# Optimization experiments

Hardware: AMD Instinct MI355X
Metric: run time of the kernel (lower is better)

Reference implementation:

```python
import jax, jax.numpy as jnp
import numpy as np

N = 50000   # nodes
E = 800000  # edges
F = 64      # node_feature_dim
H = 128     # hidden_dim


def setup_inputs() -> dict:
    key = jax.random.key(0)
    ks = jax.random.split(key, 20)
    def w(k, shape, fan_in):
        return jax.random.normal(k, shape, jnp.float32) / np.sqrt(fan_in)
    return {
        "x": jax.random.normal(ks[0], (N, F), jnp.float32),
        "edge_index": jax.random.randint(ks[1], (2, E), 0, N, jnp.int32),
        "enc_w1": w(ks[2], (F, H), F), "enc_b1": jnp.zeros((H,), jnp.float32),
        "enc_w2": w(ks[3], (H, H), H), "enc_b2": jnp.zeros((H,), jnp.float32),
        "w_c1": w(ks[4], (H, H), H), "b_c1": jnp.zeros((H,), jnp.float32),
        "w_c2": w(ks[5], (H, H), H), "b_c2": jnp.zeros((H,), jnp.float32),
        "w_c3": w(ks[6], (H, H), H), "b_c3": jnp.zeros((H,), jnp.float32),
        "dec_w1": w(ks[7], (H, H), H), "dec_b1": jnp.zeros((H,), jnp.float32),
        "dec_w2": w(ks[8], (H, F), H), "dec_b2": jnp.zeros((F,), jnp.float32),
    }


def _gcn_conv(h, W, b, src, dst, dinv):
    # PyG GCNConv: D^-1/2 (A+I) D^-1/2 (h W) + b  (self-loops already in src/dst)
    hw = h @ W                                   # [N, H]
    norm = dinv[src] * dinv[dst]                 # [E+N]
    msg = hw[src] * norm[:, None]                # gather + scale
    return jax.ops.segment_sum(msg, dst, num_segments=N) + b


def reference(x, edge_index, enc_w1, enc_b1, enc_w2, enc_b2,
              w_c1, b_c1, w_c2, b_c2, w_c3, b_c3,
              dec_w1, dec_b1, dec_w2, dec_b2):
    loop = jnp.arange(N, dtype=edge_index.dtype)
    src = jnp.concatenate([edge_index[0], loop])
    dst = jnp.concatenate([edge_index[1], loop])
    deg = jax.ops.segment_sum(jnp.ones_like(dst, jnp.float32), dst, num_segments=N)
    dinv = jax.lax.rsqrt(deg)  # deg >= 1 because of self-loops

    h = jax.nn.relu(x @ enc_w1 + enc_b1) @ enc_w2 + enc_b2  # encoder MLP
    h = jax.nn.relu(_gcn_conv(h, w_c1, b_c1, src, dst, dinv))
    h = jax.nn.relu(_gcn_conv(h, w_c2, b_c2, src, dst, dinv))
    h = jax.nn.relu(_gcn_conv(h, w_c3, b_c3, src, dst, dinv))
    # window_size == 1: chunk+cat is identity
    out = jax.nn.relu(h @ dec_w1 + dec_b1) @ dec_w2 + dec_b2  # decoder MLP
    return jax.nn.sigmoid(out)
```

## Files before the change

### kernel.cpp

```cpp
#include <hip/hip_runtime.h>
#include <stdint.h>

#define NN 50000
#define NE 800000
#define FD 64
#define HD 128
#define NBKT 196
#define BCAP 5120
#define P1E 8192

static_assert(NN % 16 == 0, "aggm16 grid is exact");

typedef __attribute__((ext_vector_type(8))) short short8;
typedef __attribute__((ext_vector_type(4))) float f32x4;

#define AS1 __attribute__((address_space(1)))
#define AS3 __attribute__((address_space(3)))

__device__ __forceinline__ float bflo(unsigned int v) {
    union { unsigned int u; float f; } c; c.u = v << 16; return c.f;
}
__device__ __forceinline__ float bfhi(unsigned int v) {
    union { unsigned int u; float f; } c; c.u = v & 0xffff0000u; return c.f;
}
__device__ __forceinline__ unsigned short f2bf(float f) {
    union { float f; unsigned int u; } c; c.f = f;
    unsigned int u = c.u;
    return (unsigned short)((u + 0x7fffu + ((u >> 16) & 1u)) >> 16);
}
__device__ __forceinline__ unsigned int pack2(float a, float b) {
    return (unsigned int)f2bf(a) | ((unsigned int)f2bf(b) << 16);
}

__global__ void wt0_k(const float* __restrict__ w0, unsigned short* __restrict__ t0) {
    int e = blockIdx.x * 256 + threadIdx.x;
    int k = e >> 7, c = e & 127;
    int gsw = (k >> 3) ^ (c & 7);
    t0[c * 64 + gsw * 8 + (k & 7)] = f2bf(w0[e]);
}

template <int K, int COLS, int EPI, bool BIAS, bool RSCALE, bool A_F32, bool OUT_F32>
__device__ __forceinline__ void mgemm_dev(
    int bid,
    const void* __restrict__ Av,
    const unsigned short* __restrict__ Wt,
    const float* __restrict__ bias,
    const float* __restrict__ dinv,
    void* __restrict__ outv, int nrows)
{
    constexpr int NB = COLS / 16;
    constexpr int KC = K / 32;
    constexpr int GMASK = (K >> 3) - 1;
    __shared__ __align__(16) unsigned char Ws8[COLS * K * 2];

    const int tid = threadIdx.x;
    const int wave = tid >> 6;
    const int lane = tid & 63;

    {
        constexpr int ROUNDS = COLS * K * 2 / 4096;
        const int gb = wave * 1024 + lane * 16;
        const int lb = wave * 1024;
        #pragma unroll
        for (int r = 0; r < ROUNDS; r++) {
            __builtin_amdgcn_global_load_lds(
                (const AS1 unsigned int*)((const unsigned char*)Wt + r * 4096 + gb),
                (AS3 unsigned int*)(Ws8 + r * 4096 + lb),
                16, 0, 0);
        }
    }

    const int m = lane & 15;
    const int q = lane >> 4;
    const int row0 = bid * 64 + wave * 16;

    f32x4 acc[NB];
    #pragma unroll
    for (int i = 0; i < NB; i++) acc[i] = (f32x4){0.f, 0.f, 0.f, 0.f};

    const bool arow_ok = !A_F32 || (row0 + m) < nrows;

    short8 af[KC];
    #pragma unroll
    for (int kc = 0; kc < KC; kc++) {
        if constexpr (A_F32) {
            const float* arowf = (const float*)Av + (size_t)(row0 + m) * K + q * 8 + kc * 32;
            float4 lo = make_float4(0.f, 0.f, 0.f, 0.f), hi = lo;
            if (arow_ok) { lo = *(const float4*)arowf; hi = *(const float4*)(arowf + 4); }
            af[kc][0] = (short)f2bf(lo.x); af[kc][1] = (short)f2bf(lo.y);
            af[kc][2] = (short)f2bf(lo.z); af[kc][3] = (short)f2bf(lo.w);
            af[kc][4] = (short)f2bf(hi.x); af[kc][5] = (short)f2bf(hi.y);
            af[kc][6] = (short)f2bf(hi.z); af[kc][7] = (short)f2bf(hi.w);
        } else {
            const unsigned short* arow = (const unsigned short*)Av + (size_t)(row0 + m) * K + q * 8 + kc * 32;
            af[kc] = *(const short8*)arow;
        }
    }
    __syncthreads();

    #pragma unroll
    for (int kc = 0; kc < KC; kc++) {
        #pragma unroll
        for (int nb = 0; nb < NB; nb++) {
            const int c = nb * 16 + m;
            const int gsw = (kc * 4 + q) ^ (c & GMASK);
            short8 bf = *(const short8*)&Ws8[(c * K + gsw * 8) * 2];
            acc[nb] = __builtin_amdgcn_mfma_f32_16x16x32_bf16(af[kc], bf, acc[nb], 0, 0, 0);
        }
    }

    float bv[NB];
    #pragma unroll
    for (int nb = 0; nb < NB; nb++) bv[nb] = BIAS ? bias[nb * 16 + m] : 0.f;

    #pragma unroll
    for (int r = 0; r < 4; r++) {
        int row = row0 + q * 4 + r;
        if (row < nrows) {
            float sc = RSCALE ? dinv[row] : 1.f;
            #pragma unroll
            for (int nb = 0; nb < NB; nb++) {
                float t = acc[nb][r];
                if (RSCALE) t *= sc;
                t += bv[nb];
                if (EPI == 1) t = fmaxf(t, 0.f);
                if (EPI == 2) t = 1.f / (1.f + __expf(-t));
                if constexpr (OUT_F32) {
                    ((float*)outv)[(size_t)row * COLS + nb * 16 + m] = t;
                } else {
                    ((unsigned short*)outv)[(size_t)row * COLS + nb * 16 + m] = f2bf(t);
                }
            }
        }
    }
}

template <int K, int COLS, int EPI, bool BIAS, bool RSCALE, bool A_F32, bool OUT_F32>
__global__ __launch_bounds__(256) void mgemm_k(
    const void* __restrict__ Av, const unsigned short* __restrict__ Wt,
    const float* __restrict__ bias, const float* __restrict__ dinv,
    void* __restrict__ outv, int nrows)
{
    mgemm_dev<K, COLS, EPI, BIAS, RSCALE, A_F32, OUT_F32>(blockIdx.x, Av, Wt, bias, dinv, outv, nrows);
}

__global__ __launch_bounds__(256) void k1_k(
    const float* __restrict__ x, const unsigned short* __restrict__ t0s,
    const float* __restrict__ enc_b1, unsigned short* __restrict__ bufA,
    const int* __restrict__ src, const int* __restrict__ dst,
    int* __restrict__ gcnt, unsigned int* __restrict__ bucket,
    const float* __restrict__ w1, const float* __restrict__ w2,
    const float* __restrict__ w3, const float* __restrict__ w4,
    const float* __restrict__ w5, const float* __restrict__ w6,
    unsigned short* __restrict__ t1, unsigned short* __restrict__ t2,
    unsigned short* __restrict__ t3, unsigned short* __restrict__ t4,
    unsigned short* __restrict__ t5, unsigned short* __restrict__ t6,
    int gb, int pb)
{
    const int b = blockIdx.x;
    if (b < gb) {
        mgemm_dev<64, 128, 1, true, false, true, false>(b, x, t0s, enc_b1, nullptr, bufA, NN);
    } else if (b < gb + pb) {
        __shared__ int lcnt[256], lsw[256], lexc[256], lofs[256], lrank[256];
        __shared__ unsigned int stage[P1E];
        const int tid = threadIdx.x;
        const int bb = b - gb;
        lcnt[tid] = 0; lrank[tid] = 0;
        __syncthreads();
        unsigned int ent[P1E / 256];
        #pragma unroll
        for (int u = 0; u < P1E / 256; u++) {
            int g = bb * P1E + u * 256 + tid;
            if (g < NE) {
                int d = dst[g], s = src[g];
                int bk = d >> 8;
                atomicAdd(&lcnt[bk], 1);
                ent[u] = (unsigned int)s | ((unsigned int)(d & 255) << 16)
                       | ((unsigned int)bk << 24);
            } else ent[u] = 0xFFFFFFFFu;
        }
        __syncthreads();
        int v = lcnt[tid];
        lsw[tid] = v; __syncthreads();
        for (int d = 1; d < 256; d <<= 1) {
            int xx = (tid >= d) ? lsw[tid - d] : 0; __syncthreads();
            lsw[tid] += xx; __syncthreads();
        }
        lexc[tid] = lsw[tid] - v;
        lofs[tid] = (v > 0) ? atomicAdd(&gcnt[tid], v) : 0;
        __syncthreads();
        #pragma unroll
        for (int u = 0; u < P1E / 256; u++) {
            if (ent[u] != 0xFFFFFFFFu) {
                int bk = ent[u] >> 24;
                int r = atomicAdd(&lrank[bk], 1);
                stage[lexc[bk] + r] = ent[u];
            }
        }
        __syncthreads();
        int cb = NE - bb * P1E; if (cb > P1E) cb = P1E;
        for (int i = tid; i < cb; i += 256) {
            unsigned int e = stage[i];
            int bk = e >> 24;
            bucket[(size_t)bk * BCAP + lofs[bk] + (i - lexc[bk])] = e;
        }
    } else {
        int b2 = b - gb - pb;
        const float* W; unsigned short* T; int C = 128;
        if      (b2 <  64) { W = w1; T = t1; }
        else if (b2 < 128) { W = w2; T = t2; b2 -= 64; }
        else if (b2 < 192) { W = w3; T = t3; b2 -= 128; }
        else if (b2 < 256) { W = w4; T = t4; b2 -= 192; }
        else if (b2 < 320) { W = w5; T = t5; b2 -= 256; }
        else               { W = w6; T = t6; b2 -= 320; C = 64; }
        int e = b2 * 256 + threadIdx.x;
        int k, c;
        if (C == 128) { k = e >> 7; c = e & 127; } else { k = e >> 6; c = e & 63; }
        int gsw = (k >> 3) ^ (c & 15);
        T[c * 128 + gsw * 8 + (k & 7)] = f2bf(W[e]);
    }
}

__global__ __launch_bounds__(256) void k2_k(
    const unsigned short* __restrict__ bufA, const unsigned short* __restrict__ t1,
    const float* __restrict__ enc_b2, unsigned short* __restrict__ bufB,
    const int* __restrict__ gcnt, const unsigned int* __restrict__ bucket,
    int* __restrict__ off, float* __restrict__ dinv,
    unsigned short* __restrict__ csr, int gb)
{
    if ((int)blockIdx.x < gb) {
        mgemm_dev<128, 128, 0, true, false, false, false>(blockIdx.x, bufA, t1, enc_b2, nullptr, bufB, NN);
    } else {
        __shared__ int lc[256], sw[256], sexc[256], lr[256], gsh[256];
        const int tid = threadIdx.x;
        const int b = blockIdx.x - gb;
        int gv = (tid < NBKT) ? gcnt[tid] : 0;
        gsh[tid] = gv; __syncthreads();
        for (int d = 1; d < 256; d <<= 1) {
            int xx = (tid >= d) ? gsh[tid - d] : 0; __syncthreads();
            gsh[tid] += xx; __syncthreads();
        }
        const int cb = gcnt[b];
        const int base = gsh[b] - cb;
        unsigned int ent[BCAP / 256];
        #pragma unroll
        for (int u = 0; u < BCAP / 256; u++) {
            int i = u * 256 + tid;
            ent[u] = (i < cb) ? bucket[(size_t)b * BCAP + i] : 0xFFFFFFFFu;
        }
        lc[tid] = 0; lr[tid] = 0;
        __syncthreads();
        #pragma unroll
        for (int u = 0; u < BCAP / 256; u++)
            if (ent[u] != 0xFFFFFFFFu) atomicAdd(&lc[(ent[u] >> 16) & 255], 1);
        __syncthreads();
        int v = lc[tid];
        int node = b * 256 + tid;
        if (node < NN) dinv[node] = rsqrtf((float)(v + 1));
        sw[tid] = v; __syncthreads();
        for (int d = 1; d < 256; d <<= 1) {
            int xx = (tid >= d) ? sw[tid - d] : 0; __syncthreads();
            sw[tid] += xx; __syncthreads();
        }
        sexc[tid] = sw[tid] - v;
        if (node < NN) off[node] = base + sexc[tid];
        if (b == NBKT - 1 && tid == 0) off[NN] = NE;
        __syncthreads();
        #pragma unroll
        for (int u = 0; u < BCAP / 256; u++) {
            if (ent[u] != 0xFFFFFFFFu) {
                int dl = (ent[u] >> 16) & 255;
                int r = atomicAdd(&lr[dl], 1);
                csr[base + sexc[dl] + r] = (unsigned short)(ent[u] & 0xffff);
            }
        }
    }
}

template <int EPI, bool BIAS, bool RSCALE>
__global__ __launch_bounds__(256) void aggm16_k(
    const uint4* __restrict__ hws, const int* __restrict__ off,
    const unsigned short* __restrict__ csr, const float* __restrict__ dinv,
    const float* __restrict__ gbias,
    const unsigned short* __restrict__ Wt,
    const float* __restrict__ obias,
    unsigned short* __restrict__ out)
{
    __shared__ __align__(16) uint4 g4[16 * 16];

    const int tid = threadIdx.x;
    const int bid = blockIdx.x;
    const int wave = tid >> 6;
    const int lane = tid & 63;
    const int m = lane & 15;
    const int q = lane >> 4;

    short8 Bf0[4], Bf1[4];
    #pragma unroll
    for (int kc = 0; kc < 4; kc++) {
        const int c0 = wave * 32 + m;
        const int c1 = c0 + 16;
        Bf0[kc] = *(const short8*)&Wt[c0 * 128 + (((kc * 4 + q) ^ (c0 & 15)) << 3)];
        Bf1[kc] = *(const short8*)&Wt[c1 * 128 + (((kc * 4 + q) ^ (c1 & 15)) << 3)];
    }

    {
        const int g = tid >> 4;
        const int l = tid & 15;
        const int row = bid * 16 + g;
        const float4 b0 = *(const float4*)(gbias + 8 * l);
        const float4 b1 = *(const float4*)(gbias + 8 * l + 4);

        uint4 v = hws[(size_t)row * 16 + l];
        float s0 = bflo(v.x), s1 = bfhi(v.x), s2 = bflo(v.y), s3 = bfhi(v.y);
        float s4 = bflo(v.z), s5 = bfhi(v.z), s6 = bflo(v.w), s7 = bfhi(v.w);
        const int je = off[row + 1];
        int j = off[row];
        for (; j + 8 <= je; j += 8) {
            uint4 t[8];
            #pragma unroll
            for (int u = 0; u < 8; u++) t[u] = hws[(size_t)csr[j + u] * 16 + l];
            #pragma unroll
            for (int u = 0; u < 8; u++) {
                s0 += bflo(t[u].x); s1 += bfhi(t[u].x);
                s2 += bflo(t[u].y); s3 += bfhi(t[u].y);
                s4 += bflo(t[u].z); s5 += bfhi(t[u].z);
                s6 += bflo(t[u].w); s7 += bfhi(t[u].w);
            }
        }
        for (; j < je; j++) {
            uint4 t = hws[(size_t)csr[j] * 16 + l];
            s0 += bflo(t.x); s1 += bfhi(t.x);
            s2 += bflo(t.y); s3 += bfhi(t.y);
            s4 += bflo(t.z); s5 += bfhi(t.z);
            s6 += bflo(t.w); s7 += bfhi(t.w);
        }
        const float di = dinv[row];
        uint4 o;
        o.x = pack2(fmaxf(fmaf(di, s0, b0.x), 0.f), fmaxf(fmaf(di, s1, b0.y), 0.f));
        o.y = pack2(fmaxf(fmaf(di, s2, b0.z), 0.f), fmaxf(fmaf(di, s3, b0.w), 0.f));
        o.z = pack2(fmaxf(fmaf(di, s4, b1.x), 0.f), fmaxf(fmaf(di, s5, b1.y), 0.f));
        o.w = pack2(fmaxf(fmaf(di, s6, b1.z), 0.f), fmaxf(fmaf(di, s7, b1.w), 0.f));
        g4[g * 16 + (l ^ g)] = o;
    }
    __syncthreads();

    f32x4 a0 = (f32x4){0.f, 0.f, 0.f, 0.f}, a1 = a0;
    #pragma unroll
    for (int kc = 0; kc < 4; kc++) {
        short8 af = *(const short8*)&g4[m * 16 + ((q + kc * 4) ^ m)];
        a0 = __builtin_amdgcn_mfma_f32_16x16x32_bf16(af, Bf0[kc], a0, 0, 0, 0);
        a1 = __builtin_amdgcn_mfma_f32_16x16x32_bf16(af, Bf1[kc], a1, 0, 0, 0);
    }

    const int c0 = wave * 32 + m;
    const int c1 = c0 + 16;
    const float bv0 = BIAS ? obias[c0] : 0.f;
    const float bv1 = BIAS ? obias[c1] : 0.f;

    #pragma unroll
    for (int r = 0; r < 4; r++) {
        const int row = bid * 16 + q * 4 + r;
        const float sc = RSCALE ? dinv[row] : 1.f;
        float t0 = a0[r], t1 = a1[r];
        if (RSCALE) { t0 *= sc; t1 *= sc; }
        t0 += bv0; t1 += bv1;
        if (EPI == 1) { t0 = fmaxf(t0, 0.f); t1 = fmaxf(t1, 0.f); }
        out[(size_t)row * 128 + c0] = f2bf(t0);
        out[(size_t)row * 128 + c1] = f2bf(t1);
    }
}

extern "C" void kernel_launch(void* const* d_in, const int* in_sizes, int n_in,
                              void* d_out, int out_size, void* d_ws, size_t ws_size,
                              hipStream_t stream)
{
    const float* x      = (const float*)d_in[0];
    const int*   ei     = (const int*)d_in[1];
    const float* enc_w1 = (const float*)d_in[2];
    const float* enc_b1 = (const float*)d_in[3];
    const float* enc_w2 = (const float*)d_in[4];
    const float* enc_b2 = (const float*)d_in[5];
    const float* w_c1   = (const float*)d_in[6];
    const float* b_c1   = (const float*)d_in[7];
    const float* w_c2   = (const float*)d_in[8];
    const float* b_c2   = (const float*)d_in[9];
    const float* w_c3   = (const float*)d_in[10];
    const float* b_c3   = (const float*)d_in[11];
    const float* dec_w1 = (const float*)d_in[12];
    const float* dec_b1 = (const float*)d_in[13];
    const float* dec_w2 = (const float*)d_in[14];
    const float* dec_b2 = (const float*)d_in[15];

    const int* src = ei;
    const int* dst = ei + NE;

    const int NP = 50048;

    char* ws = (char*)d_ws;
    size_t o = 0;
    auto alloc = [&](size_t bytes) -> void* {
        void* p = ws + o;
        o = (o + bytes + 255) & ~(size_t)255;
        return p;
    };
    int*   gcnt = (int*)alloc(256 * 4);
    int*   off  = (int*)alloc((size_t)(NN + 1) * 4);
    unsigned short* csr = (unsigned short*)alloc((size_t)NE * 2);
    unsigned int* bucket = (unsigned int*)alloc((size_t)NBKT * BCAP * 4);
    float* dinv = (float*)alloc((size_t)NN * 4);
    unsigned short* bufA = (unsigned short*)alloc((size_t)NP * HD * 2);
    unsigned short* bufB = (unsigned short*)alloc((size_t)NP * HD * 2);
    unsigned short* t0 = (unsigned short*)alloc(64 * 128 * 2);
    unsigned short* t1 = (unsigned short*)alloc(128 * 128 * 2);
    unsigned short* t2 = (unsigned short*)alloc(128 * 128 * 2);
    unsigned short* t3 = (unsigned short*)alloc(128 * 128 * 2);
    unsigned short* t4 = (unsigned short*)alloc(128 * 128 * 2);
    unsigned short* t5 = (unsigned short*)alloc(128 * 128 * 2);
    unsigned short* t6 = (unsigned short*)alloc(128 * 64 * 2);
    (void)ws_size; (void)n_in; (void)in_sizes; (void)out_size;

    hipMemsetAsync(gcnt, 0, 256 * 4, stream);

    const int PB   = (NE + P1E - 1) / P1E;
    const int GB   = NP / 64;
    const int GB16 = NN / 16;

    wt0_k<<<32, 256, 0, stream>>>(enc_w1, t0);
    k1_k<<<GB + PB + 352, 256, 0, stream>>>(x, t0, enc_b1, bufA, src, dst, gcnt, bucket,
                                            enc_w2, w_c1, w_c2, w_c3, dec_w1, dec_w2,
                                            t1, t2, t3, t4, t5, t6, GB, PB);
    k2_k<<<GB + NBKT, 256, 0, stream>>>(bufA, t1, enc_b2, bufB, gcnt, bucket,
                                        off, dinv, csr, GB);
    mgemm_k<128, 128, 0, false, true, false, false><<<GB, 256, 0, stream>>>(bufB, t2, nullptr, dinv, bufA, NN);
    aggm16_k<0, false, true><<<GB16, 256, 0, stream>>>((const uint4*)bufA, off, csr, dinv, b_c1, t3, nullptr, bufB);
    aggm16_k<0, false, true><<<GB16, 256, 0, stream>>>((const uint4*)bufB, off, csr, dinv, b_c2, t4, nullptr, bufA);
    aggm16_k<1, true, false><<<GB16, 256, 0, stream>>>((const uint4*)bufA, off, csr, dinv, b_c3, t5, dec_b1, bufB);
    mgemm_k<128, 64, 2, true, false, false, true><<<GB, 256, 0, stream>>>(bufB, t6, dec_b2, nullptr, d_out, NN);
}
```

Before: 277.9 us.

## Double-buffer neighbor gathers and stage weights to LDS in fused aggregation kernel

The aggregation+GEMM kernel now issues neighbor row gathers in two ping-pong batches of eight. Edges past the end are padded to a zeroed dummy row NN, so more loads stay in flight and the scalar tail loop is gone. The weight fragments are no longer held in registers for the whole gather phase; they are loaded asynchronously into 32 KB of LDS via global_load_lds and read just before the MFMAs. This lowers register pressure during the gather, but the extra LDS may limit occupancy, and padded loads cost extra bandwidth on low-degree rows.

```diff
diff --git a/kernel.cpp b/kernel.cpp
--- a/kernel.cpp
+++ b/kernel.cpp
@@ -32,11 +32,17 @@
     return (unsigned int)f2bf(a) | ((unsigned int)f2bf(b) << 16);
 }
 
-__global__ void wt0_k(const float* __restrict__ w0, unsigned short* __restrict__ t0) {
+__global__ void wt0_k(const float* __restrict__ w0, unsigned short* __restrict__ t0,
+                      unsigned short* __restrict__ bufA, unsigned short* __restrict__ bufB) {
     int e = blockIdx.x * 256 + threadIdx.x;
     int k = e >> 7, c = e & 127;
     int gsw = (k >> 3) ^ (c & 7);
     t0[c * 64 + gsw * 8 + (k & 7)] = f2bf(w0[e]);
+    if (blockIdx.x == 0) {
+        int t = threadIdx.x;
+        if (t < 128) bufA[(size_t)NN * 128 + t] = 0;
+        else         bufB[(size_t)NN * 128 + (t - 128)] = 0;
+    }
 }
 
 template <int K, int COLS, int EPI, bool BIAS, bool RSCALE, bool A_F32, bool OUT_F32>
@@ -286,40 +292,46 @@
     const float* __restrict__ obias,
     unsigned short* __restrict__ out)
 {
+    __shared__ __align__(16) unsigned char Ws8[128 * 128 * 2];
     __shared__ __align__(16) uint4 g4[16 * 16];
 
     const int tid = threadIdx.x;
     const int bid = blockIdx.x;
     const int wave = tid >> 6;
     const int lane = tid & 63;
-    const int m = lane & 15;
-    const int q = lane >> 4;
-
-    short8 Bf0[4], Bf1[4];
-    #pragma unroll
-    for (int kc = 0; kc < 4; kc++) {
-        const int c0 = wave * 32 + m;
-        const int c1 = c0 + 16;
-        Bf0[kc] = *(const short8*)&Wt[c0 * 128 + (((kc * 4 + q) ^ (c0 & 15)) << 3)];
-        Bf1[kc] = *(const short8*)&Wt[c1 * 128 + (((kc * 4 + q) ^ (c1 & 15)) << 3)];
+
+    {
+        const int gb = wave * 1024 + lane * 16;
+        const int lb = wave * 1024;
+        #pragma unroll
+        for (int r = 0; r < 8; r++)
+            __builtin_amdgcn_global_load_lds(
+                (const AS1 unsigned int*)((const unsigned char*)Wt + r * 4096 + gb),
+                (AS3 unsigned int*)(Ws8 + r * 4096 + lb), 16, 0, 0);
     }
 
     {
         const int g = tid >> 4;
         const int l = tid & 15;
         const int row = bid * 16 + g;
+        const int jb = off[row];
+        const int je = off[row + 1];
+
+        uint4 v = hws[(size_t)row * 16 + l];
         const float4 b0 = *(const float4*)(gbias + 8 * l);
         const float4 b1 = *(const float4*)(gbias + 8 * l + 4);
-
-        uint4 v = hws[(size_t)row * 16 + l];
         float s0 = bflo(v.x), s1 = bfhi(v.x), s2 = bflo(v.y), s3 = bfhi(v.y);
         float s4 = bflo(v.z), s5 = bfhi(v.z), s6 = bflo(v.w), s7 = bfhi(v.w);
-        const int je = off[row + 1];
-        int j = off[row];
-        for (; j + 8 <= je; j += 8) {
-            uint4 t[8];
+
+        auto issue8 = [&](uint4 (&t)[8], int j0) {
             #pragma unroll
-            for (int u = 0; u < 8; u++) t[u] = hws[(size_t)csr[j + u] * 16 + l];
+            for (int u = 0; u < 8; u++) {
+                const int gg = j0 + u;
+                const int idx = (gg < je) ? (int)csr[gg] : NN;
+                t[u] = hws[(size_t)idx * 16 + l];
+            }
+        };
+        auto consume8 = [&](uint4 (&t)[8]) {
             #pragma unroll
             for (int u = 0; u < 8; u++) {
                 s0 += bflo(t[u].x); s1 += bfhi(t[u].x);
@@ -327,14 +339,21 @@
                 s4 += bflo(t[u].z); s5 += bfhi(t[u].z);
                 s6 += bflo(t[u].w); s7 += bfhi(t[u].w);
             }
-        }
-        for (; j < je; j++) {
-            uint4 t = hws[(size_t)csr[j] * 16 + l];
-            s0 += bflo(t.x); s1 += bfhi(t.x);
-            s2 += bflo(t.y); s3 += bfhi(t.y);
-            s4 += bflo(t.z); s5 += bfhi(t.z);
-            s6 += bflo(t.w); s7 += bfhi(t.w);
-        }
+        };
+
+        const int nblk = (je - jb + 7) >> 3;
+        if (nblk > 0) {
+            uint4 ta[8], tb[8];
+            issue8(ta, jb);
+            issue8(tb, jb + 8);
+            const int npair = (nblk + 1) >> 1;
+            for (int p = 1; p < npair; p++) {
+                consume8(ta); issue8(ta, jb + p * 16);
+                consume8(tb); issue8(tb, jb + p * 16 + 8);
+            }
+            consume8(ta); consume8(tb);
+        }
+
         const float di = dinv[row];
         uint4 o;
         o.x = pack2(fmaxf(fmaf(di, s0, b0.x), 0.f), fmaxf(fmaf(di, s1, b0.y), 0.f));
@@ -345,12 +364,19 @@
     }
     __syncthreads();
 
+    const int m = lane & 15;
+    const int q = lane >> 4;
+
     f32x4 a0 = (f32x4){0.f, 0.f, 0.f, 0.f}, a1 = a0;
     #pragma unroll
     for (int kc = 0; kc < 4; kc++) {
         short8 af = *(const short8*)&g4[m * 16 + ((q + kc * 4) ^ m)];
-        a0 = __builtin_amdgcn_mfma_f32_16x16x32_bf16(af, Bf0[kc], a0, 0, 0, 0);
-        a1 = __builtin_amdgcn_mfma_f32_16x16x32_bf16(af, Bf1[kc], a1, 0, 0, 0);
+        const int c0 = wave * 32 + m;
+        const int c1 = c0 + 16;
+        short8 bf0 = *(const short8*)&Ws8[(c0 * 128 + (((kc * 4 + q) ^ (c0 & 15)) << 3)) * 2];
+        short8 bf1 = *(const short8*)&Ws8[(c1 * 128 + (((kc * 4 + q) ^ (c1 & 15)) << 3)) * 2];
+        a0 = __builtin_amdgcn_mfma_f32_16x16x32_bf16(af, bf0, a0, 0, 0, 0);
+        a1 = __builtin_amdgcn_mfma_f32_16x16x32_bf16(af, bf1, a1, 0, 0, 0);
     }
 
     const int c0 = wave * 32 + m;
@@ -406,7 +432,7 @@
     };
     int*   gcnt = (int*)alloc(256 * 4);
     int*   off  = (int*)alloc((size_t)(NN + 1) * 4);
-    unsigned short* csr = (unsigned short*)alloc((size_t)NE * 2);
+    unsigned short* csr = (unsigned short*)alloc((size_t)NE * 2 + 64);
     unsigned int* bucket = (unsigned int*)alloc((size_t)NBKT * BCAP * 4);
     float* dinv = (float*)alloc((size_t)NN * 4);
     unsigned short* bufA = (unsigned short*)alloc((size_t)NP * HD * 2);
@@ -426,7 +452,7 @@
     const int GB   = NP / 64;
     const int GB16 = NN / 16;
 
-    wt0_k<<<32, 256, 0, stream>>>(enc_w1, t0);
+    wt0_k<<<32, 256, 0, stream>>>(enc_w1, t0, bufA, bufB);
     k1_k<<<GB + PB + 352, 256, 0, stream>>>(x, t0, enc_b1, bufA, src, dst, gcnt, bucket,
                                             enc_w2, w_c1, w_c2, w_c3, dec_w1, dec_w2,
                                             t1, t2, t3, t4, t5, t6, GB, PB);
```

New measurement: 377.7 us. +35.9%, slower.

## Fuse final GCN aggregation with full decoder MLP and sigmoid into one kernel

Applied to the files above, without the earlier changes.

The last aggregation plus decoder layer-1 kernel and the separate decoder layer-2 GEMM are merged into a single kernel. It gathers neighbours, runs both decoder matmuls on MFMA with the intermediate held in LDS, applies the sigmoid and writes the fp32 output directly. This removes one kernel launch and the global write and reread of the 50000x128 bf16 intermediate. The gather code is factored into a shared device helper, and the first MFMA swaps its operands to produce a transposed tile. The cost is more LDS and registers per block, which may lower occupancy during the latency-bound gather.

```diff
diff --git a/kernel.cpp b/kernel.cpp
--- a/kernel.cpp
+++ b/kernel.cpp
@@ -277,6 +277,50 @@
     }
 }
 
+__device__ __forceinline__ void gather16_dev(
+    const uint4* __restrict__ hws, const int* __restrict__ off,
+    const unsigned short* __restrict__ csr, const float* __restrict__ dinv,
+    const float* __restrict__ gbias, uint4* __restrict__ g4, int bid, int tid)
+{
+    const int g = tid >> 4;
+    const int l = tid & 15;
+    const int row = bid * 16 + g;
+    const float4 b0 = *(const float4*)(gbias + 8 * l);
+    const float4 b1 = *(const float4*)(gbias + 8 * l + 4);
+
+    uint4 v = hws[(size_t)row * 16 + l];
+    float s0 = bflo(v.x), s1 = bfhi(v.x), s2 = bflo(v.y), s3 = bfhi(v.y);
+    float s4 = bflo(v.z), s5 = bfhi(v.z), s6 = bflo(v.w), s7 = bfhi(v.w);
+    const int je = off[row + 1];
+    int j = off[row];
+    for (; j + 8 <= je; j += 8) {
+        uint4 t[8];
+        #pragma unroll
+        for (int u = 0; u < 8; u++) t[u] = hws[(size_t)csr[j + u] * 16 + l];
+        #pragma unroll
+        for (int u = 0; u < 8; u++) {
+            s0 += bflo(t[u].x); s1 += bfhi(t[u].x);
+            s2 += bflo(t[u].y); s3 += bfhi(t[u].y);
+            s4 += bflo(t[u].z); s5 += bfhi(t[u].z);
+            s6 += bflo(t[u].w); s7 += bfhi(t[u].w);
+        }
+    }
+    for (; j < je; j++) {
+        uint4 t = hws[(size_t)csr[j] * 16 + l];
+        s0 += bflo(t.x); s1 += bfhi(t.x);
+        s2 += bflo(t.y); s3 += bfhi(t.y);
+        s4 += bflo(t.z); s5 += bfhi(t.z);
+        s6 += bflo(t.w); s7 += bfhi(t.w);
+    }
+    const float di = dinv[row];
+    uint4 o;
+    o.x = pack2(fmaxf(fmaf(di, s0, b0.x), 0.f), fmaxf(fmaf(di, s1, b0.y), 0.f));
+    o.y = pack2(fmaxf(fmaf(di, s2, b0.z), 0.f), fmaxf(fmaf(di, s3, b0.w), 0.f));
+    o.z = pack2(fmaxf(fmaf(di, s4, b1.x), 0.f), fmaxf(fmaf(di, s5, b1.y), 0.f));
+    o.w = pack2(fmaxf(fmaf(di, s6, b1.z), 0.f), fmaxf(fmaf(di, s7, b1.w), 0.f));
+    g4[g * 16 + (l ^ g)] = o;
+}
+
 template <int EPI, bool BIAS, bool RSCALE>
 __global__ __launch_bounds__(256) void aggm16_k(
     const uint4* __restrict__ hws, const int* __restrict__ off,
@@ -304,45 +348,7 @@
         Bf1[kc] = *(const short8*)&Wt[c1 * 128 + (((kc * 4 + q) ^ (c1 & 15)) << 3)];
     }
 
-    {
-        const int g = tid >> 4;
-        const int l = tid & 15;
-        const int row = bid * 16 + g;
-        const float4 b0 = *(const float4*)(gbias + 8 * l);
-        const float4 b1 = *(const float4*)(gbias + 8 * l + 4);
-
-        uint4 v = hws[(size_t)row * 16 + l];
-        float s0 = bflo(v.x), s1 = bfhi(v.x), s2 = bflo(v.y), s3 = bfhi(v.y);
-        float s4 = bflo(v.z), s5 = bfhi(v.z), s6 = bflo(v.w), s7 = bfhi(v.w);
-        const int je = off[row + 1];
-        int j = off[row];
-        for (; j + 8 <= je; j += 8) {
-            uint4 t[8];
-            #pragma unroll
-            for (int u = 0; u < 8; u++) t[u] = hws[(size_t)csr[j + u] * 16 + l];
-            #pragma unroll
-            for (int u = 0; u < 8; u++) {
-                s0 += bflo(t[u].x); s1 += bfhi(t[u].x);
-                s2 += bflo(t[u].y); s3 += bfhi(t[u].y);
-                s4 += bflo(t[u].z); s5 += bfhi(t[u].z);
-                s6 += bflo(t[u].w); s7 += bfhi(t[u].w);
-            }
-        }
-        for (; j < je; j++) {
-            uint4 t = hws[(size_t)csr[j] * 16 + l];
-            s0 += bflo(t.x); s1 += bfhi(t.x);
-            s2 += bflo(t.y); s3 += bfhi(t.y);
-            s4 += bflo(t.z); s5 += bfhi(t.z);
-            s6 += bflo(t.w); s7 += bfhi(t.w);
-        }
-        const float di = dinv[row];
-        uint4 o;
-        o.x = pack2(fmaxf(fmaf(di, s0, b0.x), 0.f), fmaxf(fmaf(di, s1, b0.y), 0.f));
-        o.y = pack2(fmaxf(fmaf(di, s2, b0.z), 0.f), fmaxf(fmaf(di, s3, b0.w), 0.f));
-        o.z = pack2(fmaxf(fmaf(di, s4, b1.x), 0.f), fmaxf(fmaf(di, s5, b1.y), 0.f));
-        o.w = pack2(fmaxf(fmaf(di, s6, b1.z), 0.f), fmaxf(fmaf(di, s7, b1.w), 0.f));
-        g4[g * 16 + (l ^ g)] = o;
-    }
+    gather16_dev(hws, off, csr, dinv, gbias, g4, bid, tid);
     __syncthreads();
 
     f32x4 a0 = (f32x4){0.f, 0.f, 0.f, 0.f}, a1 = a0;
@@ -368,6 +374,98 @@
         if (EPI == 1) { t0 = fmaxf(t0, 0.f); t1 = fmaxf(t1, 0.f); }
         out[(size_t)row * 128 + c0] = f2bf(t0);
         out[(size_t)row * 128 + c1] = f2bf(t1);
+    }
+}
+
+__global__ __launch_bounds__(256) void decf16_k(
+    const uint4* __restrict__ hws, const int* __restrict__ off,
+    const unsigned short* __restrict__ csr, const float* __restrict__ dinv,
+    const float* __restrict__ gbias,
+    const unsigned short* __restrict__ Wt1,
+    const float* __restrict__ db1,
+    const unsigned short* __restrict__ Wt2,
+    const float* __restrict__ db2,
+    float* __restrict__ outp)
+{
+    __shared__ __align__(16) uint4 g4[16 * 16];
+    __shared__ __align__(16) uint4 h4[16 * 16];
+
+    const int tid = threadIdx.x;
+    const int bid = blockIdx.x;
+    const int wave = tid >> 6;
+    const int lane = tid & 63;
+    const int m = lane & 15;
+    const int q = lane >> 4;
+
+    short8 Wf0[4], Wf1[4];
+    #pragma unroll
+    for (int kc = 0; kc < 4; kc++) {
+        const int c0 = wave * 32 + m;
+        const int c1 = c0 + 16;
+        Wf0[kc] = *(const short8*)&Wt1[c0 * 128 + (((kc * 4 + q) ^ (c0 & 15)) << 3)];
+        Wf1[kc] = *(const short8*)&Wt1[c1 * 128 + (((kc * 4 + q) ^ (c1 & 15)) << 3)];
+    }
+
+    gather16_dev(hws, off, csr, dinv, gbias, g4, bid, tid);
+    __syncthreads();
+
+    f32x4 at0 = (f32x4){0.f, 0.f, 0.f, 0.f}, at1 = at0;
+    #pragma unroll
+    for (int kc = 0; kc < 4; kc++) {
+        short8 gf = *(const short8*)&g4[m * 16 + ((q + kc * 4) ^ m)];
+        at0 = __builtin_amdgcn_mfma_f32_16x16x32_bf16(Wf0[kc], gf, at0, 0, 0, 0);
+        at1 = __builtin_amdgcn_mfma_f32_16x16x32_bf16(Wf1[kc], gf, at1, 0, 0, 0);
+    }
+
+    short8 Bf2[4];
+    #pragma unroll
+    for (int kc = 0; kc < 4; kc++) {
+        const int c = wave * 16 + m;
+        Bf2[kc] = *(const short8*)&Wt2[c * 128 + (((kc * 4 + q) ^ (c & 15)) << 3)];
+    }
+
+    {
+        uint2* h2 = (uint2*)h4;
+        {
+            const int F = wave * 32 + q * 4;
+            const float4 bb = *(const float4*)(db1 + F);
+            float v0 = fmaxf(at0[0] + bb.x, 0.f);
+            float v1 = fmaxf(at0[1] + bb.y, 0.f);
+            float v2 = fmaxf(at0[2] + bb.z, 0.f);
+            float v3 = fmaxf(at0[3] + bb.w, 0.f);
+            uint2 hv; hv.x = pack2(v0, v1); hv.y = pack2(v2, v3);
+            const int cf = wave * 4 + (q >> 1);
+            h2[m * 32 + (((cf ^ m) << 1) | (q & 1))] = hv;
+        }
+        {
+            const int F = wave * 32 + 16 + q * 4;
+            const float4 bb = *(const float4*)(db1 + F);
+            float v0 = fmaxf(at1[0] + bb.x, 0.f);
+            float v1 = fmaxf(at1[1] + bb.y, 0.f);
+            float v2 = fmaxf(at1[2] + bb.z, 0.f);
+            float v3 = fmaxf(at1[3] + bb.w, 0.f);
+            uint2 hv; hv.x = pack2(v0, v1); hv.y = pack2(v2, v3);
+            const int cf = wave * 4 + 2 + (q >> 1);
+            h2[m * 32 + (((cf ^ m) << 1) | (q & 1))] = hv;
+        }
+    }
+    __syncthreads();
+
+    f32x4 a2 = (f32x4){0.f, 0.f, 0.f, 0.f};
+    #pragma unroll
+    for (int kc = 0; kc < 4; kc++) {
+        short8 af = *(const short8*)&h4[m * 16 + ((q + kc * 4) ^ m)];
+        a2 = __builtin_amdgcn_mfma_f32_16x16x32_bf16(af, Bf2[kc], a2, 0, 0, 0);
+    }
+
+    const int c = wave * 16 + m;
+    const float bv = db2[c];
+    #pragma unroll
+    for (int r = 0; r < 4; r++) {
+        const int row = bid * 16 + q * 4 + r;
+        float t = a2[r] + bv;
+        t = 1.f / (1.f + __expf(-t));
+        outp[(size_t)row * 64 + c] = t;
     }
 }
 
@@ -435,6 +533,6 @@
     mgemm_k<128, 128, 0, false, true, false, false><<<GB, 256, 0, stream>>>(bufB, t2, nullptr, dinv, bufA, NN);
     aggm16_k<0, false, true><<<GB16, 256, 0, stream>>>((const uint4*)bufA, off, csr, dinv, b_c1, t3, nullptr, bufB);
     aggm16_k<0, false, true><<<GB16, 256, 0, stream>>>((const uint4*)bufB, off, csr, dinv, b_c2, t4, nullptr, bufA);
-    aggm16_k<1, true, false><<<GB16, 256, 0, stream>>>((const uint4*)bufA, off, csr, dinv, b_c3, t5, dec_b1, bufB);
-    mgemm_k<128, 64, 2, true, false, false, true><<<GB, 256, 0, stream>>>(bufB, t6, dec_b2, nullptr, d_out, NN);
-}
+    decf16_k<<<GB16, 256, 0, stream>>>((const uint4*)bufA, off, csr, dinv, b_c3,
+                                       t5, dec_b1, t6, dec_b2, (float*)d_out);
+}
```

After: 272.2 us. -2.1%, faster.
